# Optimization experiments

Measured on AMD Instinct MI355X. Metric: run time of the kernel, lower is better.

Reference implementation:

```python
import jax, jax.numpy as jnp
import numpy as np

NBINS = 9
CELL = 16
H, W = 256, 128          # win_size=(128,256) is (width,height)
CY, CX = H // CELL, W // CELL
BY, BX = CY - 1, CX - 1
FEAT = BY * BX * 4 * NBINS      # 3780
PAD_TO = 4096


def _hog(imgs):
    # imgs: [B, H, W, 3] float32 in [0,255]
    B = imgs.shape[0]
    x = jnp.pad(imgs, ((0, 0), (1, 1), (1, 1), (0, 0)), mode='edge')
    dx = x[:, 1:-1, 2:, :] - x[:, 1:-1, :-2, :]   # [-1,0,1] horizontal
    dy = x[:, 2:, 1:-1, :] - x[:, :-2, 1:-1, :]   # [-1,0,1] vertical
    # per-pixel: pick the channel with the largest gradient magnitude (cv2 HOG)
    mag2 = dx * dx + dy * dy
    ch = jnp.argmax(mag2, axis=-1, keepdims=True)
    dx = jnp.take_along_axis(dx, ch, axis=-1)[..., 0]
    dy = jnp.take_along_axis(dy, ch, axis=-1)[..., 0]
    mag = jnp.sqrt(dx * dx + dy * dy)
    ang = jnp.mod(jnp.arctan2(dy, dx), jnp.pi)    # unsigned gradients [0,pi)
    # bilinear orientation binning (cv2: hidx = angle*nbins/pi - 0.5)
    pos = ang * (NBINS / jnp.pi) - 0.5
    b0 = jnp.floor(pos)
    frac = pos - b0
    b0i = jnp.mod(b0.astype(jnp.int32), NBINS)
    b1i = jnp.mod(b0i + 1, NBINS)
    w0 = mag * (1.0 - frac)
    w1 = mag * frac
    # per-cell orientation histograms: [B, CY, CX, NBINS]
    hists = []
    for k in range(NBINS):
        vk = jnp.where(b0i == k, w0, 0.0) + jnp.where(b1i == k, w1, 0.0)
        vk = vk.reshape(B, CY, CELL, CX, CELL).sum(axis=(2, 4))
        hists.append(vk)
    cell_hist = jnp.stack(hists, axis=-1)
    # overlapping 2x2-cell blocks, stride = 1 cell -> [B, BY, BX, 4, NBINS]
    blk = jnp.stack([
        cell_hist[:, :-1, :-1], cell_hist[:, :-1, 1:],
        cell_hist[:, 1:, :-1], cell_hist[:, 1:, 1:]], axis=3)
    v = blk.reshape(B, BY, BX, 4 * NBINS)
    # L2-Hys block normalization (cv2: scale=1/(||v||+sz*0.1), clip 0.2, renorm)
    sz = float(4 * NBINS)
    n1 = jnp.sqrt(jnp.sum(v * v, axis=-1, keepdims=True))
    v = v / (n1 + sz * 0.1)
    v = jnp.minimum(v, 0.2)
    n2 = jnp.sqrt(jnp.sum(v * v, axis=-1, keepdims=True))
    v = v / (n2 + 1e-3)
    feat = v.reshape(B, FEAT)
    return jnp.pad(feat, ((0, 0), (0, PAD_TO - FEAT)))


def setup_inputs() -> dict:
    key = jax.random.key(0)
    k1, k2, k3 = jax.random.split(key, 3)
    B = 512
    images = jax.random.uniform(k1, (B, 3, H, W), dtype=jnp.float32) * 255.0
    targets = jax.random.randint(k2, (B,), 0, 751, dtype=jnp.int64 if jax.config.jax_enable_x64 else jnp.int32).astype(jnp.int32)
    camid = jax.random.randint(k3, (B,), 0, 8, dtype=jnp.int32)
    return {"images": images, "targets": targets, "camid": camid}


def reference(images, targets, camid):
    imgs = jnp.transpose(images, (0, 2, 3, 1))  # NCHW -> NHWC
    feat = _hog(imgs)                           # [B, 4096]
    return feat, targets, camid
```

## Files before the change

kernel.cpp:

```cpp
#include <hip/hip_runtime.h>

#define HOG_PI  3.14159265358979323846f
#define HOG_PI2 1.57079632679489661923f

typedef float f2 __attribute__((ext_vector_type(2)));

__device__ __forceinline__ float dpp_from_left(float x) {
  return __int_as_float(__builtin_amdgcn_mov_dpp(__float_as_int(x), 0x130, 0xF, 0xF, true));
}
__device__ __forceinline__ float dpp_from_right(float x) {
  return __int_as_float(__builtin_amdgcn_mov_dpp(__float_as_int(x), 0x138, 0xF, 0xF, true));
}

__device__ __forceinline__ void px_tail(
    float dxs, float dys, float g, float base, float* __restrict__ row) {
  const float mag = __builtin_amdgcn_sqrtf(g);
  const bool oct = fabsf(dys) > fabsf(dxs);
  float th = oct ? (HOG_PI2 - base) : base;
  if (dxs * dys < 0.0f) th = HOG_PI - th;
  const float pos = th * (9.0f / HOG_PI) - 0.5f;
  const float bf = floorf(pos);
  const float frac = pos - bf;
  const int b0 = (int)bf;
  const int b0i = (b0 < 0) ? 8 : b0;
  const float w0 = mag * (1.0f - frac);
  const float w1 = mag * frac;
  float* p = row + b0i;
  const float a0 = p[0];
  const float a1 = p[1];
  p[0] = a0 + w0;
  p[1] = a1 + w1;
}

__device__ __forceinline__ void accum_quad(
    const float4 c0, const float4 c1, const float4 c2,
    const float4 p0, const float4 p1, const float4 p2,
    const float4 n0, const float4 n1, const float4 n2,
    int xq, float* __restrict__ partT) {
#pragma unroll
  for (int p = 0; p < 2; ++p) {
    f2 dx[3], dy[3], g[3];
#pragma unroll
    for (int c = 0; c < 3; ++c) {
      const float4 cc = (c == 0) ? c0 : (c == 1) ? c1 : c2;
      const float4 pp = (c == 0) ? p0 : (c == 1) ? p1 : p2;
      const float4 nn = (c == 0) ? n0 : (c == 1) ? n1 : n2;
      if (p == 0) {
        float lf = dpp_from_left(cc.w);
        if (xq == 0) lf = cc.x;
        dx[c] = (f2){cc.y, cc.z} - (f2){lf, cc.x};
        dy[c] = (f2){nn.x, nn.y} - (f2){pp.x, pp.y};
      } else {
        float rf = dpp_from_right(cc.x);
        if (xq == 31) rf = cc.w;
        dx[c] = (f2){cc.w, rf} - (f2){cc.y, cc.z};
        dy[c] = (f2){nn.z, nn.w} - (f2){pp.z, pp.w};
      }
      g[c] = dx[c] * dx[c] + dy[c] * dy[c];
    }
    float dxsA = dx[0].x, dysA = dy[0].x, gA = g[0].x;
    if (g[1].x > gA) { dxsA = dx[1].x; dysA = dy[1].x; gA = g[1].x; }
    if (g[2].x > gA) { dxsA = dx[2].x; dysA = dy[2].x; gA = g[2].x; }
    float dxsB = dx[0].y, dysB = dy[0].y, gB = g[0].y;
    if (g[1].y > gB) { dxsB = dx[1].y; dysB = dy[1].y; gB = g[1].y; }
    if (g[2].y > gB) { dxsB = dx[2].y; dysB = dy[2].y; gB = g[2].y; }
    const float mnA = fminf(fabsf(dxsA), fabsf(dysA));
    const float mxA = fmaxf(fmaxf(fabsf(dxsA), fabsf(dysA)), 1e-30f);
    const float aA = mnA * __builtin_amdgcn_rcpf(mxA);
    const float mnB = fminf(fabsf(dxsB), fabsf(dysB));
    const float mxB = fmaxf(fmaxf(fabsf(dxsB), fabsf(dysB)), 1e-30f);
    const float aB = mnB * __builtin_amdgcn_rcpf(mxB);
    const f2 av = {aA, aB};
    const f2 sq = av * av;
    const f2 base =
        ((((f2)(0.0208351f) * sq - (f2)(0.0851330f)) * sq + (f2)(0.1801410f)) *
             sq - (f2)(0.3302995f)) * sq * av + (f2)(0.9998660f) * av;
    px_tail(dxsA, dysA, gA, base.x, partT);
    px_tail(dxsB, dysB, gB, base.y, partT + 10);
  }
}

__global__ __launch_bounds__(1024, 8) void hog_kernel(
    const float* __restrict__ img, const int* __restrict__ targets,
    const int* __restrict__ camid, float* __restrict__ out, int B) {
  const int b = blockIdx.x;
  const int t = threadIdx.x;
  const float* im = img + (size_t)b * (3 * 256 * 128);

  __shared__ float lds[1024 * 20];
  float* const partT = lds + t * 20;

  const int xq = t & 31;
  const int s = t >> 5;
  const int x0 = xq * 4;
  const int cx = xq >> 2;
  const int r0 = s * 8;

#pragma unroll
  for (int j = 0; j < 20; ++j) partT[j] = 0.0f;

  const float* ch0 = im;
  const float* ch1 = im + 32768;
  const float* ch2 = im + 65536;

  const int rp = (r0 == 0) ? 0 : r0 - 1;
  float4 p0 = *(const float4*)(ch0 + rp * 128 + x0);
  float4 p1 = *(const float4*)(ch1 + rp * 128 + x0);
  float4 p2 = *(const float4*)(ch2 + rp * 128 + x0);
  float4 c0 = *(const float4*)(ch0 + r0 * 128 + x0);
  float4 c1 = *(const float4*)(ch1 + r0 * 128 + x0);
  float4 c2 = *(const float4*)(ch2 + r0 * 128 + x0);

#pragma unroll 1
  for (int r = 0; r < 8; ++r) {
    const int y = r0 + r;
    const int yn = (y == 255) ? 255 : y + 1;
    const float4 n0 = *(const float4*)(ch0 + yn * 128 + x0);
    const float4 n1 = *(const float4*)(ch1 + yn * 128 + x0);
    const float4 n2 = *(const float4*)(ch2 + yn * 128 + x0);

    accum_quad(c0, c1, c2, p0, p1, p2, n0, n1, n2, xq, partT);

    p0 = c0; p1 = c1; p2 = c2;
    c0 = n0; c1 = n1; c2 = n2;
  }

  float hv[9];
#pragma unroll
  for (int k = 0; k < 9; ++k) hv[k] = partT[k] + partT[10 + k];
  hv[0] += partT[9] + partT[19];
  __syncthreads();

  float (*cellh)[8][9] = (float (*)[8][9])lds;
  const int lane = t & 63;
#pragma unroll
  for (int k = 0; k < 9; ++k) {
    float v = hv[k];
    v += __shfl_xor(v, 1, 64);
    v += __shfl_xor(v, 2, 64);
    v += __shfl_xor(v, 32, 64);
    if ((xq & 3) == 0 && lane < 32) cellh[t >> 6][cx][k] = v;
  }
  __syncthreads();

  float* outF = out + (size_t)b * 4096;
  if (t < 105) {
    const int by = t / 7;
    const int bx = t - by * 7;
    float v[36];
#pragma unroll
    for (int q = 0; q < 4; ++q) {
      const int cy = by + (q >> 1);
      const int ccx = bx + (q & 1);
#pragma unroll
      for (int k = 0; k < 9; ++k) v[q * 9 + k] = cellh[cy][ccx][k];
    }
    float ss = 0.0f;
#pragma unroll
    for (int jj = 0; jj < 36; ++jj) ss += v[jj] * v[jj];
    const float s1 = 1.0f / (sqrtf(ss) + 3.6f);
    float ss2 = 0.0f;
#pragma unroll
    for (int jj = 0; jj < 36; ++jj) {
      v[jj] = fminf(v[jj] * s1, 0.2f);
      ss2 += v[jj] * v[jj];
    }
    const float s2 = 1.0f / (sqrtf(ss2) + 1e-3f);
    float4* dst = (float4*)(outF + (by * 7 + bx) * 36);
#pragma unroll
    for (int q = 0; q < 9; ++q)
      dst[q] = make_float4(v[4 * q] * s2, v[4 * q + 1] * s2,
                           v[4 * q + 2] * s2, v[4 * q + 3] * s2);
  }
  for (int i = 3780 + t; i < 4096; i += 1024) outF[i] = 0.0f;
  if (t == 400) out[(size_t)B * 4096 + b] = (float)targets[b];
  if (t == 401) out[(size_t)B * 4096 + B + b] = (float)camid[b];
}

extern "C" void kernel_launch(void* const* d_in, const int* in_sizes, int n_in,
                              void* d_out, int out_size, void* d_ws, size_t ws_size,
                              hipStream_t stream) {
  const float* images = (const float*)d_in[0];
  const int* targets = (const int*)d_in[1];
  const int* camid = (const int*)d_in[2];
  float* out = (float*)d_out;
  const int B = in_sizes[1];
  hipLaunchKernelGGL(hog_kernel, dim3(B), dim3(1024), 0, stream,
                     images, targets, camid, out, B);
}
```

Before: 54.01 us.

## Remap threads to 2-pixel columns over full cell rows with deeper row prefetch

```diff
diff --git a/kernel.cpp b/kernel.cpp
--- a/kernel.cpp
+++ b/kernel.cpp
@@ -32,52 +32,44 @@
   p[1] = a1 + w1;
 }
 
-__device__ __forceinline__ void accum_quad(
-    const float4 c0, const float4 c1, const float4 c2,
-    const float4 p0, const float4 p1, const float4 p2,
-    const float4 n0, const float4 n1, const float4 n2,
+__device__ __forceinline__ void accum_pair(
+    const f2 c0, const f2 c1, const f2 c2,
+    const f2 p0, const f2 p1, const f2 p2,
+    const f2 n0, const f2 n1, const f2 n2,
     int xq, float* __restrict__ partT) {
+  f2 dx[3], dy[3], g[3];
 #pragma unroll
-  for (int p = 0; p < 2; ++p) {
-    f2 dx[3], dy[3], g[3];
-#pragma unroll
-    for (int c = 0; c < 3; ++c) {
-      const float4 cc = (c == 0) ? c0 : (c == 1) ? c1 : c2;
-      const float4 pp = (c == 0) ? p0 : (c == 1) ? p1 : p2;
-      const float4 nn = (c == 0) ? n0 : (c == 1) ? n1 : n2;
-      if (p == 0) {
-        float lf = dpp_from_left(cc.w);
-        if (xq == 0) lf = cc.x;
-        dx[c] = (f2){cc.y, cc.z} - (f2){lf, cc.x};
-        dy[c] = (f2){nn.x, nn.y} - (f2){pp.x, pp.y};
-      } else {
-        float rf = dpp_from_right(cc.x);
-        if (xq == 31) rf = cc.w;
-        dx[c] = (f2){cc.w, rf} - (f2){cc.y, cc.z};
-        dy[c] = (f2){nn.z, nn.w} - (f2){pp.z, pp.w};
-      }
-      g[c] = dx[c] * dx[c] + dy[c] * dy[c];
-    }
-    float dxsA = dx[0].x, dysA = dy[0].x, gA = g[0].x;
-    if (g[1].x > gA) { dxsA = dx[1].x; dysA = dy[1].x; gA = g[1].x; }
-    if (g[2].x > gA) { dxsA = dx[2].x; dysA = dy[2].x; gA = g[2].x; }
-    float dxsB = dx[0].y, dysB = dy[0].y, gB = g[0].y;
-    if (g[1].y > gB) { dxsB = dx[1].y; dysB = dy[1].y; gB = g[1].y; }
-    if (g[2].y > gB) { dxsB = dx[2].y; dysB = dy[2].y; gB = g[2].y; }
-    const float mnA = fminf(fabsf(dxsA), fabsf(dysA));
-    const float mxA = fmaxf(fmaxf(fabsf(dxsA), fabsf(dysA)), 1e-30f);
-    const float aA = mnA * __builtin_amdgcn_rcpf(mxA);
-    const float mnB = fminf(fabsf(dxsB), fabsf(dysB));
-    const float mxB = fmaxf(fmaxf(fabsf(dxsB), fabsf(dysB)), 1e-30f);
-    const float aB = mnB * __builtin_amdgcn_rcpf(mxB);
-    const f2 av = {aA, aB};
-    const f2 sq = av * av;
-    const f2 base =
-        ((((f2)(0.0208351f) * sq - (f2)(0.0851330f)) * sq + (f2)(0.1801410f)) *
-             sq - (f2)(0.3302995f)) * sq * av + (f2)(0.9998660f) * av;
-    px_tail(dxsA, dysA, gA, base.x, partT);
-    px_tail(dxsB, dysB, gB, base.y, partT + 10);
+  for (int c = 0; c < 3; ++c) {
+    const f2 cc = (c == 0) ? c0 : (c == 1) ? c1 : c2;
+    const f2 pp = (c == 0) ? p0 : (c == 1) ? p1 : p2;
+    const f2 nn = (c == 0) ? n0 : (c == 1) ? n1 : n2;
+    float lf = dpp_from_left(cc.y);
+    float rf = dpp_from_right(cc.x);
+    if (xq == 0) lf = cc.x;
+    if (xq == 63) rf = cc.y;
+    dx[c] = (f2){cc.y, rf} - (f2){lf, cc.x};
+    dy[c] = nn - pp;
+    g[c] = dx[c] * dx[c] + dy[c] * dy[c];
   }
+  float dxsA = dx[0].x, dysA = dy[0].x, gA = g[0].x;
+  if (g[1].x > gA) { dxsA = dx[1].x; dysA = dy[1].x; gA = g[1].x; }
+  if (g[2].x > gA) { dxsA = dx[2].x; dysA = dy[2].x; gA = g[2].x; }
+  float dxsB = dx[0].y, dysB = dy[0].y, gB = g[0].y;
+  if (g[1].y > gB) { dxsB = dx[1].y; dysB = dy[1].y; gB = g[1].y; }
+  if (g[2].y > gB) { dxsB = dx[2].y; dysB = dy[2].y; gB = g[2].y; }
+  const float mnA = fminf(fabsf(dxsA), fabsf(dysA));
+  const float mxA = fmaxf(fmaxf(fabsf(dxsA), fabsf(dysA)), 1e-30f);
+  const float aA = mnA * __builtin_amdgcn_rcpf(mxA);
+  const float mnB = fminf(fabsf(dxsB), fabsf(dysB));
+  const float mxB = fmaxf(fmaxf(fabsf(dxsB), fabsf(dysB)), 1e-30f);
+  const float aB = mnB * __builtin_amdgcn_rcpf(mxB);
+  const f2 av = {aA, aB};
+  const f2 sq = av * av;
+  const f2 base =
+      ((((f2)(0.0208351f) * sq - (f2)(0.0851330f)) * sq + (f2)(0.1801410f)) *
+           sq - (f2)(0.3302995f)) * sq * av + (f2)(0.9998660f) * av;
+  px_tail(dxsA, dysA, gA, base.x, partT);
+  px_tail(dxsB, dysB, gB, base.y, partT + 10);
 }
 
 __global__ __launch_bounds__(1024, 8) void hog_kernel(
@@ -90,11 +82,11 @@
   __shared__ float lds[1024 * 20];
   float* const partT = lds + t * 20;
 
-  const int xq = t & 31;
-  const int s = t >> 5;
-  const int x0 = xq * 4;
-  const int cx = xq >> 2;
-  const int r0 = s * 8;
+  const int xq = t & 63;
+  const int m = t >> 6;
+  const int x0 = xq * 2;
+  const int cx = xq >> 3;
+  const int r0 = m * 16;
 
 #pragma unroll
   for (int j = 0; j < 20; ++j) partT[j] = 0.0f;
@@ -104,25 +96,29 @@
   const float* ch2 = im + 65536;
 
   const int rp = (r0 == 0) ? 0 : r0 - 1;
-  float4 p0 = *(const float4*)(ch0 + rp * 128 + x0);
-  float4 p1 = *(const float4*)(ch1 + rp * 128 + x0);
-  float4 p2 = *(const float4*)(ch2 + rp * 128 + x0);
-  float4 c0 = *(const float4*)(ch0 + r0 * 128 + x0);
-  float4 c1 = *(const float4*)(ch1 + r0 * 128 + x0);
-  float4 c2 = *(const float4*)(ch2 + r0 * 128 + x0);
+  f2 p0 = *(const f2*)(ch0 + rp * 128 + x0);
+  f2 p1 = *(const f2*)(ch1 + rp * 128 + x0);
+  f2 p2 = *(const f2*)(ch2 + rp * 128 + x0);
+  f2 c0 = *(const f2*)(ch0 + r0 * 128 + x0);
+  f2 c1 = *(const f2*)(ch1 + r0 * 128 + x0);
+  f2 c2 = *(const f2*)(ch2 + r0 * 128 + x0);
+  f2 n0 = *(const f2*)(ch0 + (r0 + 1) * 128 + x0);
+  f2 n1 = *(const f2*)(ch1 + (r0 + 1) * 128 + x0);
+  f2 n2 = *(const f2*)(ch2 + (r0 + 1) * 128 + x0);
 
 #pragma unroll 1
-  for (int r = 0; r < 8; ++r) {
-    const int y = r0 + r;
-    const int yn = (y == 255) ? 255 : y + 1;
-    const float4 n0 = *(const float4*)(ch0 + yn * 128 + x0);
-    const float4 n1 = *(const float4*)(ch1 + yn * 128 + x0);
-    const float4 n2 = *(const float4*)(ch2 + yn * 128 + x0);
+  for (int r = 0; r < 16; ++r) {
+    const int y2 = r0 + r + 2;
+    const int yc = (y2 > 255) ? 255 : y2;
+    const f2 f0 = *(const f2*)(ch0 + yc * 128 + x0);
+    const f2 f1 = *(const f2*)(ch1 + yc * 128 + x0);
+    const f2 f2v = *(const f2*)(ch2 + yc * 128 + x0);
 
-    accum_quad(c0, c1, c2, p0, p1, p2, n0, n1, n2, xq, partT);
+    accum_pair(c0, c1, c2, p0, p1, p2, n0, n1, n2, xq, partT);
 
     p0 = c0; p1 = c1; p2 = c2;
     c0 = n0; c1 = n1; c2 = n2;
+    n0 = f0; n1 = f1; n2 = f2v;
   }
 
   float hv[9];
@@ -132,14 +128,13 @@
   __syncthreads();
 
   float (*cellh)[8][9] = (float (*)[8][9])lds;
-  const int lane = t & 63;
 #pragma unroll
   for (int k = 0; k < 9; ++k) {
     float v = hv[k];
     v += __shfl_xor(v, 1, 64);
     v += __shfl_xor(v, 2, 64);
-    v += __shfl_xor(v, 32, 64);
-    if ((xq & 3) == 0 && lane < 32) cellh[t >> 6][cx][k] = v;
+    v += __shfl_xor(v, 4, 64);
+    if ((xq & 7) == 0) cellh[m][cx][k] = v;
   }
   __syncthreads();
 
```

New measurement: 43.68 us. -19.1%, faster.
